# Performance work log

Measured on AMD Instinct MI355X. Metric: run time of the kernel, lower is better.

## Reference

```python
import jax, jax.numpy as jnp
import numpy as np

N = 100000   # nodes
E = 1600000  # edges (avg degree 16)
F = 128      # num_node_features
H = 128      # hid_size
G = 512      # num graphs in batch
C = 10       # num_classes
D = 32       # graph_degree_distribution.shape[1]
BN_EPS = 1e-5


def setup_inputs() -> dict:
    key = jax.random.key(0)
    ks = jax.random.split(key, 16)
    p = lambda k, shp: jax.random.normal(k, shp, jnp.float32) * 0.02
    x = jax.random.normal(ks[0], (N, F), jnp.float32)
    edge_index = jax.random.randint(ks[1], (2, E), 0, N)
    batch = jnp.sort(jax.random.randint(ks[2], (N,), 0, G))
    degree = jax.random.uniform(ks[3], (N,), jnp.float32) * 10.0
    return dict(
        x=x, edge_index=edge_index, batch=batch, degree=degree,
        eps1=jnp.zeros(()), W1a=p(ks[4], (F, H)), b1a=jnp.zeros(H), W1b=p(ks[5], (H, H)), b1b=jnp.zeros(H),
        g1=jnp.ones(H), be1=jnp.zeros(H),
        eps2=jnp.zeros(()), W2a=p(ks[6], (H, H)), b2a=jnp.zeros(H), W2b=p(ks[7], (H, H)), b2b=jnp.zeros(H),
        g2=jnp.ones(H), be2=jnp.zeros(H),
        Wlin1=p(ks[8], (H, H)), blin1=jnp.zeros(H),
        Wlin2=p(ks[9], (H, C)), blin2=jnp.zeros(C),
        Wlin4=p(ks[10], (H, D)), blin4=jnp.zeros(D),
        Wloss=p(ks[11], (H, 1)), bloss=jnp.zeros(1),
    )


def gin_conv(x, src, dst, eps, Wa, ba, Wb, bb, gamma, beta):
    # GINConv: MLP((1+eps)*x_i + sum_{j->i} x_j); MLP = Lin-ReLU-Lin-ReLU-BN
    agg = jax.ops.segment_sum(x[src], dst, num_segments=x.shape[0])  # [N,F] gather-scatter
    h = (1.0 + eps) * x + agg
    h = jax.nn.relu(h @ Wa + ba)
    h = jax.nn.relu(h @ Wb + bb)
    mu = h.mean(0)
    var = h.var(0)  # biased var, training-mode BN
    return gamma * (h - mu) * jax.lax.rsqrt(var + BN_EPS) + beta


def reference(x, edge_index, batch, degree,
              eps1, W1a, b1a, W1b, b1b, g1, be1,
              eps2, W2a, b2a, W2b, b2b, g2, be2,
              Wlin1, blin1, Wlin2, blin2, Wlin4, blin4, Wloss, bloss):
    src, dst = edge_index[0], edge_index[1]
    h = gin_conv(x, src, dst, eps1, W1a, b1a, W1b, b1b, g1, be1)
    h = gin_conv(h, src, dst, eps2, W2a, b2a, W2b, b2b, g2, be2)
    mse_x = h @ Wloss + bloss                       # [N,1]
    mse_loss = jnp.mean((mse_x - degree[:, None]) ** 2)
    # global_mean_pool over graphs
    sums = jax.ops.segment_sum(h, batch, num_segments=G)
    cnts = jax.ops.segment_sum(jnp.ones((h.shape[0], 1), h.dtype), batch, num_segments=G)
    g = sums / jnp.maximum(cnts, 1.0)               # [G,H]
    z = jax.nn.relu(g @ Wlin1 + blin1)              # dropout inert (eval)
    result1 = jax.nn.log_softmax(z @ Wlin2 + blin2, axis=-1)  # [G,C]
    result3 = z @ Wlin4 + blin4                      # [G,D]
    return result1, result3, mse_loss
```

## Files before the change

kernel.cpp:

```cpp
#include <hip/hip_runtime.h>
#include <hip/hip_bf16.h>

#define HF 128
#define BSH 8
#define BSZ 256
#define NBMAX 1024
#define FCAP 8192
#define HB 512

typedef __attribute__((ext_vector_type(8))) short bf16x8;
typedef __attribute__((ext_vector_type(4))) float f32x4;
typedef __attribute__((ext_vector_type(2))) float f32x2;

__device__ inline float bflo(unsigned u) { return __uint_as_float(u << 16); }
__device__ inline float bfhi(unsigned u) { return __uint_as_float(u & 0xffff0000u); }
__device__ inline unsigned short f2bf(float f) {
    unsigned u = __float_as_uint(f);
    unsigned r = (u + 0x7fffu + ((u >> 16) & 1u)) >> 16;
    return (unsigned short)r;
}
__device__ inline unsigned pack2(float a, float b) {
    return (unsigned)f2bf(a) | ((unsigned)f2bf(b) << 16);
}
__device__ inline uint2 pk8_fp8(const float* v) {
    int a = __builtin_amdgcn_cvt_pk_fp8_f32(v[0], v[1], 0, 0);
    a = __builtin_amdgcn_cvt_pk_fp8_f32(v[2], v[3], a, 1);
    int b = __builtin_amdgcn_cvt_pk_fp8_f32(v[4], v[5], 0, 0);
    b = __builtin_amdgcn_cvt_pk_fp8_f32(v[6], v[7], b, 1);
    uint2 r; r.x = (unsigned)a; r.y = (unsigned)b;
    return r;
}

__global__ __launch_bounds__(256) void init_all(
    const float* __restrict__ x, unsigned short* __restrict__ xb,
    unsigned char* __restrict__ x8, int castBlk, int nchunks,
    const float* __restrict__ w0, const float* __restrict__ w1,
    const float* __restrict__ w2, const float* __restrict__ w3,
    unsigned short* __restrict__ WtAll,
    const int* __restrict__ dst, int* __restrict__ tot, int E, int chunkH,
    const int* __restrict__ batch, int* __restrict__ gstart, int N, int Gn, int nBlocks,
    float* __restrict__ Szero, float* __restrict__ outm)
{
    __shared__ int lh[NBMAX];
    int b = blockIdx.x;
    int t = threadIdx.x;
    if (b < castBlk) {
        int i = b * 256 + t;
        if (i < nchunks) {
            float4 a = ((const float4*)x)[2 * i];
            float4 c = ((const float4*)x)[2 * i + 1];
            uint4 o;
            o.x = pack2(a.x, a.y); o.y = pack2(a.z, a.w);
            o.z = pack2(c.x, c.y); o.w = pack2(c.z, c.w);
            ((uint4*)xb)[i] = o;
            float v[8] = {a.x, a.y, a.z, a.w, c.x, c.y, c.z, c.w};
            ((uint2*)x8)[i] = pk8_fp8(v);
        }
        return;
    }
    b -= castBlk;
    if (b < 4) {
        const float* W = (b == 0) ? w0 : (b == 1) ? w1 : (b == 2) ? w2 : w3;
        unsigned short* O = WtAll + b * 16384;
        for (int idx = t; idx < 16384; idx += 256) {
            int j    = idx & 7;
            int lane = (idx >> 3) & 63;
            int fk   = idx >> 9;
            int kk = fk & 3, nt = fk >> 2;
            int m = lane & 15, quad = lane >> 4;
            int ncol = nt * 16 + m;
            int krow = kk * 32 + quad * 8 + j;
            O[idx] = f2bf(W[krow * 128 + ncol]);
        }
        return;
    }
    b -= 4;
    if (b < HB) {
        int NBl = (N + BSZ - 1) >> BSH;
        for (int i = t; i < NBl; i += 256) lh[i] = 0;
        __syncthreads();
        int beg = b * chunkH;
        int end = min(E, beg + chunkH);
        for (int e = beg + t; e < end; e += 256)
            atomicAdd(&lh[dst[e] >> BSH], 1);
        __syncthreads();
        for (int i = t; i < NBl; i += 256) {
            int c = lh[i];
            if (c) atomicAdd(&tot[i], c);
        }
        return;
    }
    b -= HB;
    if (b < nBlocks) {
        int i = b * 256 + t;
        if (i >= N) return;
        int bi = batch[i];
        int bp = (i == 0) ? -1 : batch[i - 1];
        for (int g = bp + 1; g <= bi; g++) gstart[g] = i;
        if (i == N - 1)
            for (int g = bi + 1; g <= Gn; g++) gstart[g] = N;
        return;
    }
    if (t < 2 * HF) { Szero[t] = 0.f; Szero[t + 2 * HF] = 0.f; }
    if (t == 0) outm[0] = 0.f;
}

__global__ void scanp(const int* __restrict__ tot, int* __restrict__ boff,
                      int* __restrict__ bcur, int NB, int E)
{
    __shared__ int part[256];
    int t = threadIdx.x;
    int v[4];
    int s = 0;
#pragma unroll
    for (int i = 0; i < 4; i++) {
        int idx = t * 4 + i;
        v[i] = (idx < NB) ? tot[idx] : 0;
        s += v[i];
    }
    part[t] = s;
    __syncthreads();
    for (int o = 1; o < 256; o <<= 1) {
        int y = (t >= o) ? part[t - o] : 0;
        __syncthreads();
        part[t] += y;
        __syncthreads();
    }
    int base = part[t] - s;
#pragma unroll
    for (int i = 0; i < 4; i++) {
        int idx = t * 4 + i;
        if (idx < NB) { boff[idx] = base; bcur[idx] = base; base += v[i]; }
    }
    if (t == 0) boff[NB] = E;
}

__global__ __launch_bounds__(256) void bucket_bin(
    const int* __restrict__ src, const int* __restrict__ dst,
    int* __restrict__ bcur, unsigned* __restrict__ ebuf, int E, int NB, int chunkH)
{
    __shared__ int lh[NBMAX];
    int t = threadIdx.x;
    for (int i = t; i < NB; i += 256) lh[i] = 0;
    __syncthreads();
    int beg = blockIdx.x * chunkH;
    int end = min(E, beg + chunkH);
    for (int e = beg + t; e < end; e += 256)
        atomicAdd(&lh[dst[e] >> BSH], 1);
    __syncthreads();
    for (int i = t; i < NB; i += 256) {
        int c = lh[i];
        lh[i] = c ? atomicAdd(&bcur[i], c) : 0;
    }
    __syncthreads();
    for (int e = beg + t; e < end; e += 256) {
        int d = dst[e];
        int b = d >> BSH;
        int pos = atomicAdd(&lh[b], 1);
        ebuf[pos] = ((unsigned)src[e] << BSH) | (unsigned)(d & (BSZ - 1));
    }
}

__global__ __launch_bounds__(256) void bucket_fill(
    const unsigned* __restrict__ ebuf, const int* __restrict__ boff,
    int* __restrict__ off, int* __restrict__ esrc, int N, int NB, int E)
{
    __shared__ int deg[BSZ];
    __shared__ int pref[BSZ];
    __shared__ int lcur[BSZ];
    __shared__ int lsr[FCAP];
    int b = blockIdx.x;
    int t = threadIdx.x;
    int segBeg = boff[b], segEnd = boff[b + 1];
    int segLen = segEnd - segBeg;
    int node0 = b << BSH;
    deg[t] = 0;
    __syncthreads();
    for (int i = segBeg + t; i < segEnd; i += 256)
        atomicAdd(&deg[ebuf[i] & (BSZ - 1)], 1);
    __syncthreads();
    int dv = deg[t];
    pref[t] = dv;
    __syncthreads();
    for (int o = 1; o < 256; o <<= 1) {
        int y = (t >= o) ? pref[t - o] : 0;
        __syncthreads();
        pref[t] += y;
        __syncthreads();
    }
    int excl = pref[t] - dv;
    int node = node0 + t;
    if (node < N) off[node] = segBeg + excl;
    lcur[t] = excl;
    if (b == NB - 1 && t == 0) off[N] = E;
    __syncthreads();
    if (segLen <= FCAP) {
        for (int i = segBeg + t; i < segEnd; i += 256) {
            unsigned v = ebuf[i];
            int slot = atomicAdd(&lcur[v & (BSZ - 1)], 1);
            lsr[slot] = (int)(v >> BSH);
        }
        __syncthreads();
        for (int i = t; i < segLen; i += 256) esrc[segBeg + i] = lsr[i];
    } else {
        for (int i = segBeg + t; i < segEnd; i += 256) {
            unsigned v = ebuf[i];
            int slot = atomicAdd(&lcur[v & (BSZ - 1)], 1);
            esrc[segBeg + slot] = (int)(v >> BSH);
        }
    }
}

template <bool FOLD>
__global__ __launch_bounds__(256) void gather_u(
    const unsigned short* __restrict__ xb, const unsigned char* __restrict__ x8,
    const int* __restrict__ off, const int* __restrict__ esrc,
    const float* __restrict__ epsp,
    const float* __restrict__ S1, const float* __restrict__ S2,
    const float* __restrict__ gamma, const float* __restrict__ beta, float invN,
    unsigned short* __restrict__ Uo, int N)
{
    __shared__ float lsc[HF], lsh[HF];
    int tid = threadIdx.x;
    if (FOLD) {
        if (tid < HF) {
            float mu = S1[tid] * invN;
            float var = S2[tid] * invN - mu * mu;
            float rs = rsqrtf(var + 1e-5f);
            float sc = gamma[tid] * rs;
            lsc[tid] = sc;
            lsh[tid] = beta[tid] - mu * sc;
        }
        __syncthreads();
    }
    int lane16 = tid & 15;
    int node = (blockIdx.x * 256 + tid) >> 4;
    if (node >= N) return;
    int beg = off[node], end = off[node + 1];
    float acc[8] = {0.f, 0.f, 0.f, 0.f, 0.f, 0.f, 0.f, 0.f};
    for (int j0 = beg; j0 < end; j0 += 16) {
        int myidx = (j0 + lane16 < end) ? esrc[j0 + lane16] : 0;
        int cnt = min(16, end - j0);
        for (int t = 0; t < cnt; t++) {
            int s = __shfl(myidx, t, 16);
            uint2 p = *(const uint2*)(x8 + (size_t)s * HF + lane16 * 8);
            f32x2 f0 = __builtin_amdgcn_cvt_pk_f32_fp8((int)p.x, 0);
            f32x2 f1 = __builtin_amdgcn_cvt_pk_f32_fp8((int)p.x, 1);
            f32x2 f2 = __builtin_amdgcn_cvt_pk_f32_fp8((int)p.y, 0);
            f32x2 f3 = __builtin_amdgcn_cvt_pk_f32_fp8((int)p.y, 1);
            acc[0] += f0.x; acc[1] += f0.y;
            acc[2] += f1.x; acc[3] += f1.y;
            acc[4] += f2.x; acc[5] += f2.y;
            acc[6] += f3.x; acc[7] += f3.y;
        }
    }
    float ep = 1.0f + epsp[0];
    uint4 xx = *(const uint4*)(xb + (size_t)node * HF + lane16 * 8);
    acc[0] += ep * bflo(xx.x); acc[1] += ep * bfhi(xx.x);
    acc[2] += ep * bflo(xx.y); acc[3] += ep * bfhi(xx.y);
    acc[4] += ep * bflo(xx.z); acc[5] += ep * bfhi(xx.z);
    acc[6] += ep * bflo(xx.w); acc[7] += ep * bfhi(xx.w);
    if (FOLD) {
        float cf = ep + (float)(end - beg);
        const float4 s0 = *(const float4*)(&lsc[lane16 * 8]);
        const float4 s1 = *(const float4*)(&lsc[lane16 * 8 + 4]);
        const float4 h0 = *(const float4*)(&lsh[lane16 * 8]);
        const float4 h1 = *(const float4*)(&lsh[lane16 * 8 + 4]);
        acc[0] = acc[0] * s0.x + h0.x * cf; acc[1] = acc[1] * s0.y + h0.y * cf;
        acc[2] = acc[2] * s0.z + h0.z * cf; acc[3] = acc[3] * s0.w + h0.w * cf;
        acc[4] = acc[4] * s1.x + h1.x * cf; acc[5] = acc[5] * s1.y + h1.y * cf;
        acc[6] = acc[6] * s1.z + h1.z * cf; acc[7] = acc[7] * s1.w + h1.w * cf;
    }
    uint4 o;
    o.x = pack2(acc[0], acc[1]); o.y = pack2(acc[2], acc[3]);
    o.z = pack2(acc[4], acc[5]); o.w = pack2(acc[6], acc[7]);
    *(uint4*)(Uo + (size_t)node * HF + lane16 * 8) = o;
}

__global__ __launch_bounds__(256, 4) void gemm2L(
    const unsigned short* __restrict__ U,
    const unsigned short* __restrict__ Wfa, const float* __restrict__ ba,
    const unsigned short* __restrict__ Wfb, const float* __restrict__ bb,
    unsigned short* __restrict__ out, unsigned char* __restrict__ out8,
    float* __restrict__ S1, float* __restrict__ S2, int n)
{
    __shared__ __align__(16) unsigned short lT[8192];
    __shared__ float lS1[HF], lS2[HF];
    int tid = threadIdx.x;
    int w = tid >> 6, lane = tid & 63;
    int m = lane & 15, quad = lane >> 4;
    int tile = (blockIdx.x << 2) | w;
    int ntiles = (n + 15) >> 4;
    bool active = tile < ntiles;

    if (tid < HF) { lS1[tid] = 0.f; lS2[tid] = 0.f; }
    __syncthreads();

    if (active) {
        unsigned short* lTw = lT + w * 2048;
        int swzA = (m & 7) << 3;
        int row0 = tile << 4;

        int ar = row0 + m; if (ar >= n) ar = n - 1;
        const unsigned short* up = U + (size_t)ar * HF + quad * 8;
        bf16x8 aF[4];
#pragma unroll
        for (int kk = 0; kk < 4; kk++) aF[kk] = *(const bf16x8*)(up + kk * 32);

        float bav[8], bbv[8];
#pragma unroll
        for (int nt = 0; nt < 8; nt++) { bav[nt] = ba[nt * 16 + m]; bbv[nt] = bb[nt * 16 + m]; }

        const bf16x8* __restrict__ Ba = (const bf16x8*)Wfa;
        const bf16x8* __restrict__ Bb = (const bf16x8*)Wfb;

        f32x4 acc[8];
#pragma unroll
        for (int nt = 0; nt < 8; nt++) acc[nt] = (f32x4){0.f, 0.f, 0.f, 0.f};
#pragma unroll
        for (int nt = 0; nt < 8; nt++) {
#pragma unroll
            for (int kk = 0; kk < 4; kk++) {
                bf16x8 b = Ba[(((nt << 2) | kk) << 6) | lane];
                acc[nt] = __builtin_amdgcn_mfma_f32_16x16x32_bf16(aF[kk], b, acc[nt], 0, 0, 0);
            }
        }
#pragma unroll
        for (int nt = 0; nt < 8; nt++) {
#pragma unroll
            for (int r = 0; r < 4; r++) {
                int row = (quad << 2) | r;
                lTw[(row << 7) | ((nt * 16 + m) ^ ((row & 7) << 3))] =
                    f2bf(fmaxf(acc[nt][r] + bav[nt], 0.f));
            }
        }
        bf16x8 a2[4];
#pragma unroll
        for (int kk = 0; kk < 4; kk++)
            a2[kk] = *(const bf16x8*)(&lTw[(m << 7) | (((kk << 5) | (quad << 3)) ^ swzA)]);
#pragma unroll
        for (int nt = 0; nt < 8; nt++) acc[nt] = (f32x4){0.f, 0.f, 0.f, 0.f};
#pragma unroll
        for (int nt = 0; nt < 8; nt++) {
#pragma unroll
            for (int kk = 0; kk < 4; kk++) {
                bf16x8 b = Bb[(((nt << 2) | kk) << 6) | lane];
                acc[nt] = __builtin_amdgcn_mfma_f32_16x16x32_bf16(a2[kk], b, acc[nt], 0, 0, 0);
            }
        }
#pragma unroll
        for (int nt = 0; nt < 8; nt++) {
            float cs = 0.f, cq = 0.f;
#pragma unroll
            for (int r = 0; r < 4; r++) {
                int row = (quad << 2) | r;
                float v = fmaxf(acc[nt][r] + bbv[nt], 0.f);
                lTw[(row << 7) | ((nt * 16 + m) ^ ((row & 7) << 3))] = f2bf(v);
                if (row0 + row < n) { cs += v; cq += v * v; }
            }
            cs += __shfl_down(cs, 32); cs += __shfl_down(cs, 16);
            cq += __shfl_down(cq, 32); cq += __shfl_down(cq, 16);
            if (quad == 0) {
                atomicAdd(&lS1[nt * 16 + m], cs);
                atomicAdd(&lS2[nt * 16 + m], cq);
            }
        }
#pragma unroll
        for (int i = 0; i < 4; i++) {
            int chunk = (i << 6) | lane;
            int row = chunk >> 4, c16 = chunk & 15;
            int grow = row0 + row;
            if (grow < n) {
                uint4 v = *(const uint4*)(&lTw[(row << 7) | (((c16 << 3) ^ ((row & 7) << 3)))]);
                *(uint4*)(out + (size_t)grow * HF + (c16 << 3)) = v;
                if (out8) {
                    float f[8] = {bflo(v.x), bfhi(v.x), bflo(v.y), bfhi(v.y),
                                  bflo(v.z), bfhi(v.z), bflo(v.w), bfhi(v.w)};
                    *(uint2*)(out8 + (size_t)grow * HF + (c16 << 3)) = pk8_fp8(f);
                }
            }
        }
    }
    __syncthreads();
    if (tid < HF) {
        atomicAdd(&S1[tid], lS1[tid]);
        atomicAdd(&S2[tid], lS2[tid]);
    }
}

__global__ __launch_bounds__(512) void pool_tail(
    const unsigned short* __restrict__ h2raw,
    const float* __restrict__ S1, const float* __restrict__ S2,
    const float* __restrict__ gamma, const float* __restrict__ beta, float invN,
    const int* __restrict__ gstart, const float* __restrict__ W,
    const float* __restrict__ bias,
    const float* __restrict__ Wloss, const float* __restrict__ blossp,
    const float* __restrict__ degree,
    const float* __restrict__ W2, const float* __restrict__ b2,
    const float* __restrict__ W4, const float* __restrict__ b4,
    float* __restrict__ out1, float* __restrict__ out3,
    float* __restrict__ outm, int C_, int D_)
{
    __shared__ float lsc[HF], lsh[HF];
    __shared__ float red[8][HF];
    __shared__ float gv[HF];
    __shared__ float part[4][HF];
    __shared__ float wred[8];
    __shared__ float zz[HF];
    __shared__ float logits[16];
    __shared__ float lse_s;
    int gid = blockIdx.x;
    int t = threadIdx.x;
    if (t < HF) {
        float mu = S1[t] * invN;
        float var = S2[t] * invN - mu * mu;
        float rs = rsqrtf(var + 1e-5f);
        float sc = gamma[t] * rs;
        lsc[t] = sc;
        lsh[t] = beta[t] - mu * sc;
    }
    __syncthreads();
    int c2 = t & 63;
    int rg = t >> 6;
    int b = gstart[gid], e = gstart[gid + 1];
    float wla = lsc[2 * c2] * Wloss[2 * c2];
    float wlb = lsc[2 * c2 + 1] * Wloss[2 * c2 + 1];
    float c0l = lsh[2 * c2] * Wloss[2 * c2] + lsh[2 * c2 + 1] * Wloss[2 * c2 + 1];
    float bl = blossp[0];
    float s0 = 0.f, s1 = 0.f, macc = 0.f;
    for (int r = b + rg; r < e; r += 8) {
        unsigned u = *(const unsigned*)(h2raw + (size_t)r * HF + c2 * 2);
        float v0 = bflo(u), v1 = bfhi(u);
        s0 += v0; s1 += v1;
        float m = v0 * wla + v1 * wlb + c0l;
#pragma unroll
        for (int o = 32; o > 0; o >>= 1) m += __shfl_down(m, o);
        if (c2 == 0) {
            float d = m + bl - degree[r];
            macc += d * d;
        }
    }
    red[rg][c2 * 2] = s0;
    red[rg][c2 * 2 + 1] = s1;
    if (c2 == 0) wred[rg] = macc;
    __syncthreads();
    if (t < HF) {
        float s = red[0][t] + red[1][t] + red[2][t] + red[3][t]
                + red[4][t] + red[5][t] + red[6][t] + red[7][t];
        gv[t] = (e > b) ? lsc[t] * (s / (float)(e - b)) + lsh[t] : 0.f;
    }
    __syncthreads();
    int c = t & 127, kg = t >> 7;
    float a = 0.f;
#pragma unroll 8
    for (int k = kg * 32; k < kg * 32 + 32; k++) a += gv[k] * W[(size_t)k * HF + c];
    part[kg][c] = a;
    __syncthreads();
    if (t < HF) {
        float aa = part[0][t] + part[1][t] + part[2][t] + part[3][t] + bias[t];
        zz[t] = fmaxf(aa, 0.f);
    }
    if (t == 0) {
        float ps = wred[0] + wred[1] + wred[2] + wred[3]
                 + wred[4] + wred[5] + wred[6] + wred[7];
        atomicAdd(outm, ps * invN);
    }
    __syncthreads();
    if (t < C_) {
        float aa = b2[t];
        for (int k = 0; k < HF; k++) aa += zz[k] * W2[(size_t)k * C_ + t];
        logits[t] = aa;
    }
    __syncthreads();
    if (t == 0) {
        float mx = -1e30f;
        for (int i = 0; i < C_; i++) mx = fmaxf(mx, logits[i]);
        float s = 0.f;
        for (int i = 0; i < C_; i++) s += expf(logits[i] - mx);
        lse_s = mx + logf(s);
    }
    __syncthreads();
    if (t < C_) out1[(size_t)gid * C_ + t] = logits[t] - lse_s;
    if (t < D_) {
        float aa = b4[t];
        for (int k = 0; k < HF; k++) aa += zz[k] * W4[(size_t)k * D_ + t];
        out3[(size_t)gid * D_ + t] = aa;
    }
}

extern "C" void kernel_launch(void* const* d_in, const int* in_sizes, int n_in,
                              void* d_out, int out_size, void* d_ws, size_t ws_size,
                              hipStream_t stream)
{
    const float* x      = (const float*)d_in[0];
    const int*   ei     = (const int*)d_in[1];
    const int*   batch  = (const int*)d_in[2];
    const float* degree = (const float*)d_in[3];
    const float* eps1   = (const float*)d_in[4];
    const float* W1a    = (const float*)d_in[5];
    const float* b1a    = (const float*)d_in[6];
    const float* W1b    = (const float*)d_in[7];
    const float* b1b    = (const float*)d_in[8];
    const float* g1     = (const float*)d_in[9];
    const float* be1    = (const float*)d_in[10];
    const float* eps2   = (const float*)d_in[11];
    const float* W2a    = (const float*)d_in[12];
    const float* b2a    = (const float*)d_in[13];
    const float* W2b    = (const float*)d_in[14];
    const float* b2b    = (const float*)d_in[15];
    const float* g2     = (const float*)d_in[16];
    const float* be2    = (const float*)d_in[17];
    const float* Wlin1  = (const float*)d_in[18];
    const float* blin1  = (const float*)d_in[19];
    const float* Wlin2  = (const float*)d_in[20];
    const float* blin2  = (const float*)d_in[21];
    const float* Wlin4  = (const float*)d_in[22];
    const float* blin4  = (const float*)d_in[23];
    const float* Wloss  = (const float*)d_in[24];
    const float* bloss  = (const float*)d_in[25];

    const int N  = in_sizes[0] / HF;
    const int E  = in_sizes[1] / 2;
    const int C_ = in_sizes[21];
    const int D_ = in_sizes[23];
    const int Gn = (out_size - 1) / (C_ + D_);
    const int NB = (N + BSZ - 1) >> BSH;

    const int* src = ei;
    const int* dst = ei + E;

    size_t NH = (size_t)N * HF;
    char* p = (char*)d_ws;
    unsigned short* xb  = (unsigned short*)p; p += NH * 2;
    unsigned short* U   = (unsigned short*)p; p += NH * 2;
    unsigned short* Hp1 = (unsigned short*)p; p += NH * 2;
    unsigned short* Hp2 = (unsigned short*)p; p += NH * 2;
    unsigned char*  x8  = (unsigned char*)p; p += NH;
    unsigned char*  h8  = (unsigned char*)p; p += NH;
    unsigned short* WtAll = (unsigned short*)p; p += 4 * 16384 * 2;
    float* S1a  = (float*)p; p += HF * 4;
    float* S2a  = (float*)p; p += HF * 4;
    float* S1b  = (float*)p; p += HF * 4;
    float* S2b  = (float*)p; p += HF * 4;
    int* gstart = (int*)p; p += (Gn + 1) * 4;
    int* boff   = (int*)p; p += (NBMAX + 1) * 4;
    int* bcur   = (int*)p; p += NBMAX * 4;
    int* tot    = (int*)p; p += NBMAX * 4;
    int* off    = (int*)p; p += (N + 1) * 4;
    int* esrc   = (int*)p; p += E * 4;
    unsigned* ebuf = (unsigned*)p; p += E * 4;

    unsigned short* Wt1a = WtAll;
    unsigned short* Wt1b = WtAll + 16384;
    unsigned short* Wt2a = WtAll + 32768;
    unsigned short* Wt2b = WtAll + 49152;

    float* out1 = (float*)d_out;
    float* out3 = out1 + (size_t)Gn * C_;
    float* outm = out3 + (size_t)Gn * D_;

    int nchunks  = (int)(NH / 8);
    int castBlk  = (nchunks + 255) / 256;
    int nBlocks  = (N + 255) / 256;
    int gatherBlk = (N * 16 + 255) / 256;
    int ntiles   = (N + 15) / 16;
    int gemmBlk  = (ntiles + 3) / 4;
    int chunkH   = (E + HB - 1) / HB;
    float invN = 1.0f / (float)N;

    int initBlk = castBlk + 4 + HB + nBlocks + 1;

    hipMemsetAsync(tot, 0, (size_t)NB * sizeof(int), stream);
    init_all<<<initBlk, 256, 0, stream>>>(x, xb, x8, castBlk, nchunks,
                                          W1a, W1b, W2a, W2b, WtAll,
                                          dst, tot, E, chunkH,
                                          batch, gstart, N, Gn, nBlocks,
                                          S1a, outm);
    scanp<<<1, 256, 0, stream>>>(tot, boff, bcur, NB, E);
    bucket_bin<<<HB, 256, 0, stream>>>(src, dst, bcur, ebuf, E, NB, chunkH);
    bucket_fill<<<NB, 256, 0, stream>>>(ebuf, boff, off, esrc, N, NB, E);
    gather_u<false><<<gatherBlk, 256, 0, stream>>>(xb, x8, off, esrc, eps1,
                                                   nullptr, nullptr, nullptr, nullptr, 0.f, U, N);
    gemm2L<<<gemmBlk, 256, 0, stream>>>(U, Wt1a, b1a, Wt1b, b1b, Hp1, h8, S1a, S2a, N);
    gather_u<true><<<gatherBlk, 256, 0, stream>>>(Hp1, h8, off, esrc, eps2,
                                                  S1a, S2a, g1, be1, invN, U, N);
    gemm2L<<<gemmBlk, 256, 0, stream>>>(U, Wt2a, b2a, Wt2b, b2b, Hp2, nullptr, S1b, S2b, N);
    pool_tail<<<Gn, 512, 0, stream>>>(Hp2, S1b, S2b, g2, be2, invN, gstart,
                                      Wlin1, blin1, Wloss, bloss, degree,
                                      Wlin2, blin2, Wlin4, blin4,
                                      out1, out3, outm, C_, D_);
}
```

Measured before the change: 479.2 us.

## Fuse neighbor gather with two-layer MLP GEMM per GIN layer

Merges the per-layer gather kernel and the MFMA GEMM kernel into one kernel. Each 256-thread block gathers 64 nodes straight into a swizzled LDS tile, and each wave then runs both MLP layers on its own 16 rows. This removes the global U intermediate (a full N×128 bf16 write and read per layer) and two kernel launches. In exchange, each 16-lane group now handles 4 nodes one after another, which cuts the number of gather loads in flight and may lower latency hiding during the irregular gather.

```diff
diff --git a/kernel.cpp b/kernel.cpp
--- a/kernel.cpp
+++ b/kernel.cpp
@@ -212,172 +212,165 @@
 }
 
 template <bool FOLD>
-__global__ __launch_bounds__(256) void gather_u(
-    const unsigned short* __restrict__ xb, const unsigned char* __restrict__ x8,
+__global__ __launch_bounds__(256, 4) void layer_fused(
+    const unsigned short* __restrict__ xbSelf, const unsigned char* __restrict__ x8,
     const int* __restrict__ off, const int* __restrict__ esrc,
     const float* __restrict__ epsp,
-    const float* __restrict__ S1, const float* __restrict__ S2,
+    const float* __restrict__ S1in, const float* __restrict__ S2in,
     const float* __restrict__ gamma, const float* __restrict__ beta, float invN,
-    unsigned short* __restrict__ Uo, int N)
-{
+    const unsigned short* __restrict__ Wfa, const float* __restrict__ ba,
+    const unsigned short* __restrict__ Wfb, const float* __restrict__ bb,
+    unsigned short* __restrict__ out, unsigned char* __restrict__ out8,
+    float* __restrict__ S1, float* __restrict__ S2, int n)
+{
+    __shared__ __align__(16) unsigned short lU[8192];
+    __shared__ float lS1[HF], lS2[HF];
     __shared__ float lsc[HF], lsh[HF];
     int tid = threadIdx.x;
-    if (FOLD) {
-        if (tid < HF) {
-            float mu = S1[tid] * invN;
-            float var = S2[tid] * invN - mu * mu;
+    if (tid < HF) {
+        lS1[tid] = 0.f; lS2[tid] = 0.f;
+        if (FOLD) {
+            float mu = S1in[tid] * invN;
+            float var = S2in[tid] * invN - mu * mu;
             float rs = rsqrtf(var + 1e-5f);
             float sc = gamma[tid] * rs;
             lsc[tid] = sc;
             lsh[tid] = beta[tid] - mu * sc;
         }
-        __syncthreads();
-    }
+    }
+    __syncthreads();
+
     int lane16 = tid & 15;
-    int node = (blockIdx.x * 256 + tid) >> 4;
-    if (node >= N) return;
-    int beg = off[node], end = off[node + 1];
-    float acc[8] = {0.f, 0.f, 0.f, 0.f, 0.f, 0.f, 0.f, 0.f};
-    for (int j0 = beg; j0 < end; j0 += 16) {
-        int myidx = (j0 + lane16 < end) ? esrc[j0 + lane16] : 0;
-        int cnt = min(16, end - j0);
-        for (int t = 0; t < cnt; t++) {
-            int s = __shfl(myidx, t, 16);
-            uint2 p = *(const uint2*)(x8 + (size_t)s * HF + lane16 * 8);
-            f32x2 f0 = __builtin_amdgcn_cvt_pk_f32_fp8((int)p.x, 0);
-            f32x2 f1 = __builtin_amdgcn_cvt_pk_f32_fp8((int)p.x, 1);
-            f32x2 f2 = __builtin_amdgcn_cvt_pk_f32_fp8((int)p.y, 0);
-            f32x2 f3 = __builtin_amdgcn_cvt_pk_f32_fp8((int)p.y, 1);
-            acc[0] += f0.x; acc[1] += f0.y;
-            acc[2] += f1.x; acc[3] += f1.y;
-            acc[4] += f2.x; acc[5] += f2.y;
-            acc[6] += f3.x; acc[7] += f3.y;
-        }
-    }
+    int g = tid >> 4;
+    int base = blockIdx.x * 64;
     float ep = 1.0f + epsp[0];
-    uint4 xx = *(const uint4*)(xb + (size_t)node * HF + lane16 * 8);
-    acc[0] += ep * bflo(xx.x); acc[1] += ep * bfhi(xx.x);
-    acc[2] += ep * bflo(xx.y); acc[3] += ep * bfhi(xx.y);
-    acc[4] += ep * bflo(xx.z); acc[5] += ep * bfhi(xx.z);
-    acc[6] += ep * bflo(xx.w); acc[7] += ep * bfhi(xx.w);
-    if (FOLD) {
-        float cf = ep + (float)(end - beg);
-        const float4 s0 = *(const float4*)(&lsc[lane16 * 8]);
-        const float4 s1 = *(const float4*)(&lsc[lane16 * 8 + 4]);
-        const float4 h0 = *(const float4*)(&lsh[lane16 * 8]);
-        const float4 h1 = *(const float4*)(&lsh[lane16 * 8 + 4]);
-        acc[0] = acc[0] * s0.x + h0.x * cf; acc[1] = acc[1] * s0.y + h0.y * cf;
-        acc[2] = acc[2] * s0.z + h0.z * cf; acc[3] = acc[3] * s0.w + h0.w * cf;
-        acc[4] = acc[4] * s1.x + h1.x * cf; acc[5] = acc[5] * s1.y + h1.y * cf;
-        acc[6] = acc[6] * s1.z + h1.z * cf; acc[7] = acc[7] * s1.w + h1.w * cf;
-    }
-    uint4 o;
-    o.x = pack2(acc[0], acc[1]); o.y = pack2(acc[2], acc[3]);
-    o.z = pack2(acc[4], acc[5]); o.w = pack2(acc[6], acc[7]);
-    *(uint4*)(Uo + (size_t)node * HF + lane16 * 8) = o;
-}
-
-__global__ __launch_bounds__(256, 4) void gemm2L(
-    const unsigned short* __restrict__ U,
-    const unsigned short* __restrict__ Wfa, const float* __restrict__ ba,
-    const unsigned short* __restrict__ Wfb, const float* __restrict__ bb,
-    unsigned short* __restrict__ out, unsigned char* __restrict__ out8,
-    float* __restrict__ S1, float* __restrict__ S2, int n)
-{
-    __shared__ __align__(16) unsigned short lT[8192];
-    __shared__ float lS1[HF], lS2[HF];
-    int tid = threadIdx.x;
+
+    for (int i = 0; i < 4; i++) {
+        int urow = g * 4 + i;
+        int node = base + urow;
+        float acc[8] = {0.f, 0.f, 0.f, 0.f, 0.f, 0.f, 0.f, 0.f};
+        if (node < n) {
+            int beg = off[node], end = off[node + 1];
+            for (int j0 = beg; j0 < end; j0 += 16) {
+                int myidx = (j0 + lane16 < end) ? esrc[j0 + lane16] : 0;
+                int cnt = min(16, end - j0);
+                for (int t = 0; t < cnt; t++) {
+                    int s = __shfl(myidx, t, 16);
+                    uint2 p = *(const uint2*)(x8 + (size_t)s * HF + lane16 * 8);
+                    f32x2 f0 = __builtin_amdgcn_cvt_pk_f32_fp8((int)p.x, 0);
+                    f32x2 f1 = __builtin_amdgcn_cvt_pk_f32_fp8((int)p.x, 1);
+                    f32x2 f2 = __builtin_amdgcn_cvt_pk_f32_fp8((int)p.y, 0);
+                    f32x2 f3 = __builtin_amdgcn_cvt_pk_f32_fp8((int)p.y, 1);
+                    acc[0] += f0.x; acc[1] += f0.y;
+                    acc[2] += f1.x; acc[3] += f1.y;
+                    acc[4] += f2.x; acc[5] += f2.y;
+                    acc[6] += f3.x; acc[7] += f3.y;
+                }
+            }
+            uint4 xx = *(const uint4*)(xbSelf + (size_t)node * HF + lane16 * 8);
+            acc[0] += ep * bflo(xx.x); acc[1] += ep * bfhi(xx.x);
+            acc[2] += ep * bflo(xx.y); acc[3] += ep * bfhi(xx.y);
+            acc[4] += ep * bflo(xx.z); acc[5] += ep * bfhi(xx.z);
+            acc[6] += ep * bflo(xx.w); acc[7] += ep * bfhi(xx.w);
+            if (FOLD) {
+                float cf = ep + (float)(end - beg);
+                const float4 s0 = *(const float4*)(&lsc[lane16 * 8]);
+                const float4 s1 = *(const float4*)(&lsc[lane16 * 8 + 4]);
+                const float4 h0 = *(const float4*)(&lsh[lane16 * 8]);
+                const float4 h1 = *(const float4*)(&lsh[lane16 * 8 + 4]);
+                acc[0] = acc[0] * s0.x + h0.x * cf; acc[1] = acc[1] * s0.y + h0.y * cf;
+                acc[2] = acc[2] * s0.z + h0.z * cf; acc[3] = acc[3] * s0.w + h0.w * cf;
+                acc[4] = acc[4] * s1.x + h1.x * cf; acc[5] = acc[5] * s1.y + h1.y * cf;
+                acc[6] = acc[6] * s1.z + h1.z * cf; acc[7] = acc[7] * s1.w + h1.w * cf;
+            }
+        }
+        uint4 o;
+        o.x = pack2(acc[0], acc[1]); o.y = pack2(acc[2], acc[3]);
+        o.z = pack2(acc[4], acc[5]); o.w = pack2(acc[6], acc[7]);
+        *(uint4*)(&lU[(urow << 7) | ((lane16 * 8) ^ ((urow & 7) << 3))]) = o;
+    }
+
     int w = tid >> 6, lane = tid & 63;
     int m = lane & 15, quad = lane >> 4;
-    int tile = (blockIdx.x << 2) | w;
-    int ntiles = (n + 15) >> 4;
-    bool active = tile < ntiles;
-
-    if (tid < HF) { lS1[tid] = 0.f; lS2[tid] = 0.f; }
-    __syncthreads();
-
-    if (active) {
-        unsigned short* lTw = lT + w * 2048;
-        int swzA = (m & 7) << 3;
-        int row0 = tile << 4;
-
-        int ar = row0 + m; if (ar >= n) ar = n - 1;
-        const unsigned short* up = U + (size_t)ar * HF + quad * 8;
-        bf16x8 aF[4];
-#pragma unroll
-        for (int kk = 0; kk < 4; kk++) aF[kk] = *(const bf16x8*)(up + kk * 32);
-
-        float bav[8], bbv[8];
-#pragma unroll
-        for (int nt = 0; nt < 8; nt++) { bav[nt] = ba[nt * 16 + m]; bbv[nt] = bb[nt * 16 + m]; }
-
-        const bf16x8* __restrict__ Ba = (const bf16x8*)Wfa;
-        const bf16x8* __restrict__ Bb = (const bf16x8*)Wfb;
-
-        f32x4 acc[8];
-#pragma unroll
-        for (int nt = 0; nt < 8; nt++) acc[nt] = (f32x4){0.f, 0.f, 0.f, 0.f};
-#pragma unroll
-        for (int nt = 0; nt < 8; nt++) {
-#pragma unroll
-            for (int kk = 0; kk < 4; kk++) {
-                bf16x8 b = Ba[(((nt << 2) | kk) << 6) | lane];
-                acc[nt] = __builtin_amdgcn_mfma_f32_16x16x32_bf16(aF[kk], b, acc[nt], 0, 0, 0);
-            }
-        }
-#pragma unroll
-        for (int nt = 0; nt < 8; nt++) {
-#pragma unroll
-            for (int r = 0; r < 4; r++) {
-                int row = (quad << 2) | r;
-                lTw[(row << 7) | ((nt * 16 + m) ^ ((row & 7) << 3))] =
-                    f2bf(fmaxf(acc[nt][r] + bav[nt], 0.f));
-            }
-        }
-        bf16x8 a2[4];
-#pragma unroll
-        for (int kk = 0; kk < 4; kk++)
-            a2[kk] = *(const bf16x8*)(&lTw[(m << 7) | (((kk << 5) | (quad << 3)) ^ swzA)]);
-#pragma unroll
-        for (int nt = 0; nt < 8; nt++) acc[nt] = (f32x4){0.f, 0.f, 0.f, 0.f};
-#pragma unroll
-        for (int nt = 0; nt < 8; nt++) {
-#pragma unroll
-            for (int kk = 0; kk < 4; kk++) {
-                bf16x8 b = Bb[(((nt << 2) | kk) << 6) | lane];
-                acc[nt] = __builtin_amdgcn_mfma_f32_16x16x32_bf16(a2[kk], b, acc[nt], 0, 0, 0);
-            }
-        }
-#pragma unroll
-        for (int nt = 0; nt < 8; nt++) {
-            float cs = 0.f, cq = 0.f;
-#pragma unroll
-            for (int r = 0; r < 4; r++) {
-                int row = (quad << 2) | r;
-                float v = fmaxf(acc[nt][r] + bbv[nt], 0.f);
-                lTw[(row << 7) | ((nt * 16 + m) ^ ((row & 7) << 3))] = f2bf(v);
-                if (row0 + row < n) { cs += v; cq += v * v; }
-            }
-            cs += __shfl_down(cs, 32); cs += __shfl_down(cs, 16);
-            cq += __shfl_down(cq, 32); cq += __shfl_down(cq, 16);
-            if (quad == 0) {
-                atomicAdd(&lS1[nt * 16 + m], cs);
-                atomicAdd(&lS2[nt * 16 + m], cq);
-            }
-        }
-#pragma unroll
-        for (int i = 0; i < 4; i++) {
-            int chunk = (i << 6) | lane;
-            int row = chunk >> 4, c16 = chunk & 15;
-            int grow = row0 + row;
-            if (grow < n) {
-                uint4 v = *(const uint4*)(&lTw[(row << 7) | (((c16 << 3) ^ ((row & 7) << 3)))]);
-                *(uint4*)(out + (size_t)grow * HF + (c16 << 3)) = v;
-                if (out8) {
-                    float f[8] = {bflo(v.x), bfhi(v.x), bflo(v.y), bfhi(v.y),
-                                  bflo(v.z), bfhi(v.z), bflo(v.w), bfhi(v.w)};
-                    *(uint2*)(out8 + (size_t)grow * HF + (c16 << 3)) = pk8_fp8(f);
-                }
+    unsigned short* lTw = lU + w * 2048;
+    int swzA = (m & 7) << 3;
+    int row0 = base + w * 16;
+
+    bf16x8 aF[4];
+#pragma unroll
+    for (int kk = 0; kk < 4; kk++)
+        aF[kk] = *(const bf16x8*)(&lTw[(m << 7) | (((kk << 5) | (quad << 3)) ^ swzA)]);
+
+    float bav[8], bbv[8];
+#pragma unroll
+    for (int nt = 0; nt < 8; nt++) { bav[nt] = ba[nt * 16 + m]; bbv[nt] = bb[nt * 16 + m]; }
+
+    const bf16x8* __restrict__ Ba = (const bf16x8*)Wfa;
+    const bf16x8* __restrict__ Bb = (const bf16x8*)Wfb;
+
+    f32x4 acc[8];
+#pragma unroll
+    for (int nt = 0; nt < 8; nt++) acc[nt] = (f32x4){0.f, 0.f, 0.f, 0.f};
+#pragma unroll
+    for (int nt = 0; nt < 8; nt++) {
+#pragma unroll
+        for (int kk = 0; kk < 4; kk++) {
+            bf16x8 b = Ba[(((nt << 2) | kk) << 6) | lane];
+            acc[nt] = __builtin_amdgcn_mfma_f32_16x16x32_bf16(aF[kk], b, acc[nt], 0, 0, 0);
+        }
+    }
+#pragma unroll
+    for (int nt = 0; nt < 8; nt++) {
+#pragma unroll
+        for (int r = 0; r < 4; r++) {
+            int row = (quad << 2) | r;
+            lTw[(row << 7) | ((nt * 16 + m) ^ ((row & 7) << 3))] =
+                f2bf(fmaxf(acc[nt][r] + bav[nt], 0.f));
+        }
+    }
+    bf16x8 a2[4];
+#pragma unroll
+    for (int kk = 0; kk < 4; kk++)
+        a2[kk] = *(const bf16x8*)(&lTw[(m << 7) | (((kk << 5) | (quad << 3)) ^ swzA)]);
+#pragma unroll
+    for (int nt = 0; nt < 8; nt++) acc[nt] = (f32x4){0.f, 0.f, 0.f, 0.f};
+#pragma unroll
+    for (int nt = 0; nt < 8; nt++) {
+#pragma unroll
+        for (int kk = 0; kk < 4; kk++) {
+            bf16x8 b = Bb[(((nt << 2) | kk) << 6) | lane];
+            acc[nt] = __builtin_amdgcn_mfma_f32_16x16x32_bf16(a2[kk], b, acc[nt], 0, 0, 0);
+        }
+    }
+#pragma unroll
+    for (int nt = 0; nt < 8; nt++) {
+        float cs = 0.f, cq = 0.f;
+#pragma unroll
+        for (int r = 0; r < 4; r++) {
+            int row = (quad << 2) | r;
+            float v = fmaxf(acc[nt][r] + bbv[nt], 0.f);
+            lTw[(row << 7) | ((nt * 16 + m) ^ ((row & 7) << 3))] = f2bf(v);
+            if (row0 + row < n) { cs += v; cq += v * v; }
+        }
+        cs += __shfl_down(cs, 32); cs += __shfl_down(cs, 16);
+        cq += __shfl_down(cq, 32); cq += __shfl_down(cq, 16);
+        if (quad == 0) {
+            atomicAdd(&lS1[nt * 16 + m], cs);
+            atomicAdd(&lS2[nt * 16 + m], cq);
+        }
+    }
+#pragma unroll
+    for (int i = 0; i < 4; i++) {
+        int chunk = (i << 6) | lane;
+        int row = chunk >> 4, c16 = chunk & 15;
+        int grow = row0 + row;
+        if (grow < n) {
+            uint4 v = *(const uint4*)(&lTw[(row << 7) | (((c16 << 3) ^ ((row & 7) << 3)))]);
+            *(uint4*)(out + (size_t)grow * HF + (c16 << 3)) = v;
+            if (out8) {
+                float f[8] = {bflo(v.x), bfhi(v.x), bflo(v.y), bfhi(v.y),
+                              bflo(v.z), bfhi(v.z), bflo(v.w), bfhi(v.w)};
+                *(uint2*)(out8 + (size_t)grow * HF + (c16 << 3)) = pk8_fp8(f);
             }
         }
     }
@@ -532,7 +525,6 @@
     size_t NH = (size_t)N * HF;
     char* p = (char*)d_ws;
     unsigned short* xb  = (unsigned short*)p; p += NH * 2;
-    unsigned short* U   = (unsigned short*)p; p += NH * 2;
     unsigned short* Hp1 = (unsigned short*)p; p += NH * 2;
     unsigned short* Hp2 = (unsigned short*)p; p += NH * 2;
     unsigned char*  x8  = (unsigned char*)p; p += NH;
@@ -562,9 +554,7 @@
     int nchunks  = (int)(NH / 8);
     int castBlk  = (nchunks + 255) / 256;
     int nBlocks  = (N + 255) / 256;
-    int gatherBlk = (N * 16 + 255) / 256;
-    int ntiles   = (N + 15) / 16;
-    int gemmBlk  = (ntiles + 3) / 4;
+    int fusedBlk = (N + 63) / 64;
     int chunkH   = (E + HB - 1) / HB;
     float invN = 1.0f / (float)N;
 
@@ -579,12 +569,14 @@
     scanp<<<1, 256, 0, stream>>>(tot, boff, bcur, NB, E);
     bucket_bin<<<HB, 256, 0, stream>>>(src, dst, bcur, ebuf, E, NB, chunkH);
     bucket_fill<<<NB, 256, 0, stream>>>(ebuf, boff, off, esrc, N, NB, E);
-    gather_u<false><<<gatherBlk, 256, 0, stream>>>(xb, x8, off, esrc, eps1,
-                                                   nullptr, nullptr, nullptr, nullptr, 0.f, U, N);
-    gemm2L<<<gemmBlk, 256, 0, stream>>>(U, Wt1a, b1a, Wt1b, b1b, Hp1, h8, S1a, S2a, N);
-    gather_u<true><<<gatherBlk, 256, 0, stream>>>(Hp1, h8, off, esrc, eps2,
-                                                  S1a, S2a, g1, be1, invN, U, N);
-    gemm2L<<<gemmBlk, 256, 0, stream>>>(U, Wt2a, b2a, Wt2b, b2b, Hp2, nullptr, S1b, S2b, N);
+    layer_fused<false><<<fusedBlk, 256, 0, stream>>>(
+        xb, x8, off, esrc, eps1,
+        nullptr, nullptr, nullptr, nullptr, 0.f,
+        Wt1a, b1a, Wt1b, b1b, Hp1, h8, S1a, S2a, N);
+    layer_fused<true><<<fusedBlk, 256, 0, stream>>>(
+        Hp1, h8, off, esrc, eps2,
+        S1a, S2a, g1, be1, invN,
+        Wt2a, b2a, Wt2b, b2b, Hp2, nullptr, S1b, S2b, N);
     pool_tail<<<Gn, 512, 0, stream>>>(Hp2, S1b, S2b, g2, be2, invN, gstart,
                                       Wlin1, blin1, Wloss, bloss, degree,
                                       Wlin2, blin2, Wlin4, blin4,
```

New measurement: 514.8 us. 1.07x slower.
